# Kernel optimization log

Hardware: AMD Instinct MI355X
Metric: run time of the kernel (lower is better)

## Reference

```python
import jax, jax.numpy as jnp
import numpy as np

D = 16  # feature (height) dim fixed by nn.Linear(16,16)

def setup_inputs() -> dict:
    key = jax.random.key(0)
    ks = jax.random.split(key, 7)
    B, C = 32, 1024
    inp = jax.random.normal(ks[0], (B, C, D), dtype=jnp.float32)
    s = 1.0 / np.sqrt(D)
    Wq = jax.random.uniform(ks[1], (D, D), jnp.float32, -s, s)
    bq = jax.random.uniform(ks[2], (D,), jnp.float32, -s, s)
    Wk = jax.random.uniform(ks[3], (D, D), jnp.float32, -s, s)
    bk = jax.random.uniform(ks[4], (D,), jnp.float32, -s, s)
    Wv = jax.random.uniform(ks[5], (D, D), jnp.float32, -s, s)
    bv = jax.random.uniform(ks[6], (D,), jnp.float32, -s, s)
    return {"input": inp, "Wq": Wq, "bq": bq, "Wk": Wk, "bk": bk, "Wv": Wv, "bv": bv}

def reference(input, Wq, bq, Wk, bk, Wv, bv):
    # torch Linear: y = x @ W.T + b
    Q = jnp.einsum('bcd,ed->bce', input, Wq) + bq  # [B,C,16]
    K = jnp.einsum('bcd,ed->bce', input, Wk) + bk
    V = jnp.einsum('bcd,ed->bce', input, Wv) + bv
    W = jnp.einsum('bqd,bkd->bqk', Q, K)           # [B,C,C], unscaled
    W = jax.nn.softmax(W, axis=2)
    att = jnp.einsum('bqk,bkd->bqd', W, V)         # [B,C,16]
    return att * input                              # elementwise gate
```

## Files before the change

kernel.cpp:

```cpp
#include <hip/hip_runtime.h>
#include <math.h>

#define DD 16
#define CC 1024
#define BB 32
#define QT 128
#define KT 256

__global__ __launch_bounds__(256) void qkv_kernel(
    const float* __restrict__ x,
    const float* __restrict__ Wq, const float* __restrict__ bq,
    const float* __restrict__ Wk, const float* __restrict__ bk,
    const float* __restrict__ Wv, const float* __restrict__ bv,
    float* __restrict__ Q, float* __restrict__ K, float* __restrict__ V)
{
    __shared__ float xs[256 * DD];
    const int tid = threadIdx.x;
    const int m = blockIdx.y;
    const float* W    = (m == 0) ? Wq : (m == 1) ? Wk : Wv;
    const float* bias = (m == 0) ? bq : (m == 1) ? bk : bv;
    float*       O    = (m == 0) ? Q  : (m == 1) ? K  : V;

    const long base4 = (long)blockIdx.x * 256 * 4;
    const float4* x4 = (const float4*)x;
    float4* xs4 = (float4*)xs;
#pragma unroll
    for (int i = 0; i < 4; ++i)
        xs4[i * 256 + tid] = x4[base4 + i * 256 + tid];
    __syncthreads();

    float xr[16];
#pragma unroll
    for (int i = 0; i < 4; ++i) {
        float4 t = xs4[tid * 4 + i];
        xr[i*4+0] = t.x; xr[i*4+1] = t.y; xr[i*4+2] = t.z; xr[i*4+3] = t.w;
    }

    const long row = (long)blockIdx.x * 256 + tid;
    float4* O4 = (float4*)O;
#pragma unroll
    for (int g = 0; g < 4; ++g) {
        float o[4];
#pragma unroll
        for (int j = 0; j < 4; ++j) {
            const int e = g * 4 + j;
            float a = bias[e];
            const float* w = W + e * 16;
#pragma unroll
            for (int d = 0; d < 16; ++d) a = fmaf(xr[d], w[d], a);
            o[j] = a;
        }
        float4 ov; ov.x = o[0]; ov.y = o[1]; ov.z = o[2]; ov.w = o[3];
        O4[row * 4 + g] = ov;
    }
}

__global__ __launch_bounds__(512, 2) void attn_kernel(
    const float* __restrict__ Q, const float* __restrict__ K,
    const float* __restrict__ V, const float* __restrict__ x,
    float* __restrict__ out)
{
    __shared__ float smem[8192 + 512];
    float4* Ks4 = (float4*)smem;
    float4* Vs4 = (float4*)(smem + 4096);

    const int tid = threadIdx.x;
    const int q32 = tid & 31;
    const int ks  = tid >> 5;
    const int b   = blockIdx.y;
    const int qbase = blockIdx.x * QT;

    const float4* Q4 = (const float4*)Q;
    float qr[4][16];
#pragma unroll
    for (int qb = 0; qb < 4; ++qb) {
        const long row = (long)b * CC + qbase + qb * 32 + q32;
#pragma unroll
        for (int i = 0; i < 4; ++i) {
            float4 t = Q4[row * 4 + i];
            qr[qb][i*4+0] = t.x; qr[qb][i*4+1] = t.y;
            qr[qb][i*4+2] = t.z; qr[qb][i*4+3] = t.w;
        }
    }

    float lsum[4];
    float acc[4][16];
#pragma unroll
    for (int qb = 0; qb < 4; ++qb) {
        lsum[qb] = 0.f;
#pragma unroll
        for (int d = 0; d < 16; ++d) acc[qb][d] = 0.f;
    }

    const float4* K4 = (const float4*)K;
    const float4* V4 = (const float4*)V;

    for (int t = 0; t < 4; ++t) {
        const long tb4 = ((long)b * CC + t * KT) * 4;
        __syncthreads();
        Ks4[tid]       = K4[tb4 + tid];
        Ks4[tid + 512] = K4[tb4 + tid + 512];
        Vs4[tid]       = V4[tb4 + tid];
        Vs4[tid + 512] = V4[tb4 + tid + 512];
        __syncthreads();

#pragma unroll 4
        for (int kk = 0; kk < 16; ++kk) {
            const int kl = (kk << 4) + ks;
            const float4 ka = Ks4[kl * 4 + 0];
            const float4 kb = Ks4[kl * 4 + 1];
            const float4 kc = Ks4[kl * 4 + 2];
            const float4 kd = Ks4[kl * 4 + 3];
            float kr[16];
            kr[0]=ka.x; kr[1]=ka.y; kr[2]=ka.z; kr[3]=ka.w;
            kr[4]=kb.x; kr[5]=kb.y; kr[6]=kb.z; kr[7]=kb.w;
            kr[8]=kc.x; kr[9]=kc.y; kr[10]=kc.z; kr[11]=kc.w;
            kr[12]=kd.x; kr[13]=kd.y; kr[14]=kd.z; kr[15]=kd.w;

            float p[4];
#pragma unroll
            for (int qb = 0; qb < 4; ++qb) {
                float s = qr[qb][0] * kr[0];
#pragma unroll
                for (int d = 1; d < 16; ++d) s = fmaf(qr[qb][d], kr[d], s);
                p[qb] = __expf(s);
                lsum[qb] += p[qb];
            }

            const float4 va = Vs4[kl * 4 + 0];
            const float4 vb = Vs4[kl * 4 + 1];
            const float4 vc = Vs4[kl * 4 + 2];
            const float4 vd = Vs4[kl * 4 + 3];
            float vr[16];
            vr[0]=va.x; vr[1]=va.y; vr[2]=va.z; vr[3]=va.w;
            vr[4]=vb.x; vr[5]=vb.y; vr[6]=vb.z; vr[7]=vb.w;
            vr[8]=vc.x; vr[9]=vc.y; vr[10]=vc.z; vr[11]=vc.w;
            vr[12]=vd.x; vr[13]=vd.y; vr[14]=vd.z; vr[15]=vd.w;
#pragma unroll
            for (int qb = 0; qb < 4; ++qb)
#pragma unroll
                for (int d = 0; d < 16; ++d)
                    acc[qb][d] = fmaf(p[qb], vr[d], acc[qb][d]);
        }
    }

    float* As = smem;
    float* Ls = smem + 8192;
    float4* As4 = (float4*)As;
    const float4* x4 = (const float4*)x;
    float4* out4 = (float4*)out;

#pragma unroll
    for (int qb = 0; qb < 4; ++qb) {
        __syncthreads();
#pragma unroll
        for (int i = 0; i < 4; ++i) {
            float4 t4;
            t4.x = acc[qb][i*4+0]; t4.y = acc[qb][i*4+1];
            t4.z = acc[qb][i*4+2]; t4.w = acc[qb][i*4+3];
            As4[tid * 4 + i] = t4;
        }
        Ls[tid] = lsum[qb];
        __syncthreads();

        if (tid < 128) {
            const int qq = tid >> 2;
            const int dg = tid & 3;
            float L = 0.f;
            float4 o; o.x = 0.f; o.y = 0.f; o.z = 0.f; o.w = 0.f;
#pragma unroll
            for (int s = 0; s < 16; ++s) {
                L += Ls[s * 32 + qq];
                float4 a = As4[(s * 32 + qq) * 4 + dg];
                o.x += a.x; o.y += a.y; o.z += a.z; o.w += a.w;
            }
            const float invL = 1.f / L;
            const long orow = (long)b * CC + qbase + qb * 32 + qq;
            const float4 xg = x4[orow * 4 + dg];
            float4 r;
            r.x = o.x * invL * xg.x;
            r.y = o.y * invL * xg.y;
            r.z = o.z * invL * xg.z;
            r.w = o.w * invL * xg.w;
            out4[orow * 4 + dg] = r;
        }
    }
}

extern "C" void kernel_launch(void* const* d_in, const int* in_sizes, int n_in,
                              void* d_out, int out_size, void* d_ws, size_t ws_size,
                              hipStream_t stream) {
    const float* x  = (const float*)d_in[0];
    const float* Wq = (const float*)d_in[1];
    const float* bq = (const float*)d_in[2];
    const float* Wk = (const float*)d_in[3];
    const float* bk = (const float*)d_in[4];
    const float* Wv = (const float*)d_in[5];
    const float* bv = (const float*)d_in[6];
    float* out = (float*)d_out;

    const long n = (long)BB * CC * DD;
    float* Q = (float*)d_ws;
    float* K = Q + n;
    float* V = K + n;

    qkv_kernel<<<dim3((BB * CC) / 256, 3), dim3(256), 0, stream>>>(
        x, Wq, bq, Wk, bk, Wv, bv, Q, K, V);

    attn_kernel<<<dim3(CC / QT, BB), dim3(512), 0, stream>>>(Q, K, V, x, out);
}
```

Baseline: 108.5 us.

## Stream K/V directly from global memory with register prefetch instead of LDS tiles

Removes the shared-memory staging of K and V tiles and the per-tile barriers in the attention loop. Each thread now reads its K/V row straight from global memory, which is wave-uniform since all lanes share the same ks, and prefetches the next row into registers while computing the current one. This trades LDS traffic and syncs for uncached-broadcast global/L1 loads and adds about 32 live registers, which may hurt occupancy under the (512,2) launch bounds.

```diff
diff --git a/kernel.cpp b/kernel.cpp
--- a/kernel.cpp
+++ b/kernel.cpp
@@ -5,7 +5,6 @@
 #define CC 1024
 #define BB 32
 #define QT 128
-#define KT 256
 
 __global__ __launch_bounds__(256) void qkv_kernel(
     const float* __restrict__ x,
@@ -61,8 +60,6 @@
     float* __restrict__ out)
 {
     __shared__ float smem[8192 + 512];
-    float4* Ks4 = (float4*)smem;
-    float4* Vs4 = (float4*)(smem + 4096);
 
     const int tid = threadIdx.x;
     const int q32 = tid & 31;
@@ -92,56 +89,48 @@
         for (int d = 0; d < 16; ++d) acc[qb][d] = 0.f;
     }
 
-    const float4* K4 = (const float4*)K;
-    const float4* V4 = (const float4*)V;
-
-    for (int t = 0; t < 4; ++t) {
-        const long tb4 = ((long)b * CC + t * KT) * 4;
-        __syncthreads();
-        Ks4[tid]       = K4[tb4 + tid];
-        Ks4[tid + 512] = K4[tb4 + tid + 512];
-        Vs4[tid]       = V4[tb4 + tid];
-        Vs4[tid + 512] = V4[tb4 + tid + 512];
-        __syncthreads();
+    const float4* Kg = (const float4*)K + (long)b * CC * 4;
+    const float4* Vg = (const float4*)V + (long)b * CC * 4;
+
+    float4 k0 = Kg[ks*4+0], k1 = Kg[ks*4+1], k2 = Kg[ks*4+2], k3 = Kg[ks*4+3];
+    float4 v0 = Vg[ks*4+0], v1 = Vg[ks*4+1], v2 = Vg[ks*4+2], v3 = Vg[ks*4+3];
 
 #pragma unroll 4
-        for (int kk = 0; kk < 16; ++kk) {
-            const int kl = (kk << 4) + ks;
-            const float4 ka = Ks4[kl * 4 + 0];
-            const float4 kb = Ks4[kl * 4 + 1];
-            const float4 kc = Ks4[kl * 4 + 2];
-            const float4 kd = Ks4[kl * 4 + 3];
-            float kr[16];
-            kr[0]=ka.x; kr[1]=ka.y; kr[2]=ka.z; kr[3]=ka.w;
-            kr[4]=kb.x; kr[5]=kb.y; kr[6]=kb.z; kr[7]=kb.w;
-            kr[8]=kc.x; kr[9]=kc.y; kr[10]=kc.z; kr[11]=kc.w;
-            kr[12]=kd.x; kr[13]=kd.y; kr[14]=kd.z; kr[15]=kd.w;
-
-            float p[4];
-#pragma unroll
-            for (int qb = 0; qb < 4; ++qb) {
-                float s = qr[qb][0] * kr[0];
-#pragma unroll
-                for (int d = 1; d < 16; ++d) s = fmaf(qr[qb][d], kr[d], s);
-                p[qb] = __expf(s);
-                lsum[qb] += p[qb];
-            }
-
-            const float4 va = Vs4[kl * 4 + 0];
-            const float4 vb = Vs4[kl * 4 + 1];
-            const float4 vc = Vs4[kl * 4 + 2];
-            const float4 vd = Vs4[kl * 4 + 3];
-            float vr[16];
-            vr[0]=va.x; vr[1]=va.y; vr[2]=va.z; vr[3]=va.w;
-            vr[4]=vb.x; vr[5]=vb.y; vr[6]=vb.z; vr[7]=vb.w;
-            vr[8]=vc.x; vr[9]=vc.y; vr[10]=vc.z; vr[11]=vc.w;
-            vr[12]=vd.x; vr[13]=vd.y; vr[14]=vd.z; vr[15]=vd.w;
-#pragma unroll
-            for (int qb = 0; qb < 4; ++qb)
-#pragma unroll
-                for (int d = 0; d < 16; ++d)
-                    acc[qb][d] = fmaf(p[qb], vr[d], acc[qb][d]);
-        }
+    for (int kk = 0; kk < 64; ++kk) {
+        float4 nk0, nk1, nk2, nk3, nv0, nv1, nv2, nv3;
+        if (kk + 1 < 64) {
+            const int kn = ((kk + 1) << 4) + ks;
+            nk0 = Kg[kn*4+0]; nk1 = Kg[kn*4+1]; nk2 = Kg[kn*4+2]; nk3 = Kg[kn*4+3];
+            nv0 = Vg[kn*4+0]; nv1 = Vg[kn*4+1]; nv2 = Vg[kn*4+2]; nv3 = Vg[kn*4+3];
+        }
+
+        float kr[16], vr[16];
+        kr[0]=k0.x; kr[1]=k0.y; kr[2]=k0.z; kr[3]=k0.w;
+        kr[4]=k1.x; kr[5]=k1.y; kr[6]=k1.z; kr[7]=k1.w;
+        kr[8]=k2.x; kr[9]=k2.y; kr[10]=k2.z; kr[11]=k2.w;
+        kr[12]=k3.x; kr[13]=k3.y; kr[14]=k3.z; kr[15]=k3.w;
+        vr[0]=v0.x; vr[1]=v0.y; vr[2]=v0.z; vr[3]=v0.w;
+        vr[4]=v1.x; vr[5]=v1.y; vr[6]=v1.z; vr[7]=v1.w;
+        vr[8]=v2.x; vr[9]=v2.y; vr[10]=v2.z; vr[11]=v2.w;
+        vr[12]=v3.x; vr[13]=v3.y; vr[14]=v3.z; vr[15]=v3.w;
+
+        float p[4];
+#pragma unroll
+        for (int qb = 0; qb < 4; ++qb) {
+            float s = qr[qb][0] * kr[0];
+#pragma unroll
+            for (int d = 1; d < 16; ++d) s = fmaf(qr[qb][d], kr[d], s);
+            p[qb] = __expf(s);
+            lsum[qb] += p[qb];
+        }
+#pragma unroll
+        for (int qb = 0; qb < 4; ++qb)
+#pragma unroll
+            for (int d = 0; d < 16; ++d)
+                acc[qb][d] = fmaf(p[qb], vr[d], acc[qb][d]);
+
+        k0 = nk0; k1 = nk1; k2 = nk2; k3 = nk3;
+        v0 = nv0; v1 = nv1; v2 = nv2; v3 = nv3;
     }
 
     float* As = smem;
```

New measurement: 223.2 us. 2.06x slower.
